# Performance work log

Measured on AMD Instinct MI355X. Metric: run time of the kernel, lower is better.

## Reference

```python
import jax, jax.numpy as jnp
import numpy as np

DT = 0.1
NUM_STEPS = 10
THRESHOLD = 0.3


def setup_inputs() -> dict:
    key = jax.random.key(0)
    k1, k2, k3 = jax.random.split(key, 3)
    B, T, D = 8, 4096, 1024
    L, O = 3, 4
    x = jax.random.normal(k1, (B, T, D), dtype=jnp.float32)
    # nn.Linear(dim, O, bias=False) weights per level, stacked: (L, O, D)
    W = jax.random.normal(k2, (L, O, D), dtype=jnp.float32) / np.sqrt(D)
    # omegas init: randn*0.1 + freq_scales[min(i,2)], freq_scales=[4.0,2.0,0.6]
    freq = jnp.array([4.0, 2.0, 0.6], dtype=jnp.float32)[:, None]
    omegas = jax.random.normal(k3, (L, O), dtype=jnp.float32) * 0.1 + freq
    # coupling strengths: 1.0 + i*0.5
    Ks = 1.0 + 0.5 * jnp.arange(L, dtype=jnp.float32)
    return {"x": x, "W": W, "omegas": omegas, "Ks": Ks}


def reference(x, W, omegas, Ks):
    B, T, D = x.shape
    L, O, _ = W.shape
    two_pi = 2.0 * jnp.pi

    # per-level projection: (L, B, T, O)
    proj = jnp.einsum('btd,lod->lbto', x, W)
    # initial phases from adjacent oscillator ratio
    phases = jnp.arctan2(proj, jnp.roll(proj, 1, axis=-1) + 1e-8) % two_pi

    om = omegas[:, None, None, :]      # (L,1,1,O)
    K = Ks[:, None, None, None]        # (L,1,1,1)

    def step(ph, _):
        # mean phase over time dim per oscillator (circular mean)
        mean_phase = jnp.arctan2(jnp.sin(ph).mean(axis=2, keepdims=True),
                                 jnp.cos(ph).mean(axis=2, keepdims=True))
        coupling = K * jnp.sin(mean_phase - ph) / T
        return (ph + DT * (om + coupling)) % two_pi, None

    phases, _ = jax.lax.scan(step, phases, None, length=NUM_STEPS)

    s = jnp.sin(phases)
    c = jnp.cos(phases)
    # global coherence: |mean_t exp(i*phi)| averaged over oscillators -> (B, L)
    level_coherences = jnp.sqrt(s.mean(axis=2) ** 2 + c.mean(axis=2) ** 2).mean(-1).T

    # sliding window-of-3 coherence along T -> (L, B, T-2)
    ms = (s[:, :, :-2] + s[:, :, 1:-1] + s[:, :, 2:]) / 3.0
    mc = (c[:, :, :-2] + c[:, :, 1:-1] + c[:, :, 2:]) / 3.0
    coh = jnp.sqrt(ms ** 2 + mc ** 2).mean(-1)
    # local-minimum dip detection: boundary at coherence index i+1 (i in 1..T-5)
    cond = (coh[..., 1:-1] < coh[..., :-2] - THRESHOLD) & \
           (coh[..., 1:-1] < coh[..., 2:] - THRESHOLD)      # (L, B, T-4)
    boundary_mask = jnp.pad(cond, ((0, 0), (0, 0), (2, 0)))   # (L, B, T-2)

    return phases, level_coherences, boundary_mask
```

## Files before the change

### kernel.cpp

```cpp
#include <hip/hip_runtime.h>
#include <math.h>

#define NB 8
#define NT 4096
#define ND 1024
#define NL 3
#define NO 4
#define NLO 12
#define NROWS (NB * NT)
#define TWO_PI_D 6.283185307179586476925286766559
#define DT_D 0.1
#define NSTEPS 10
#define THRESH_D 0.3

typedef double f64x4 __attribute__((ext_vector_type(4)));

__global__ __launch_bounds__(256) void k_wprep(const float* __restrict__ W,
                                               double* __restrict__ wsWt)
{
    int i = blockIdx.x * 256 + threadIdx.x;
    if (i < 1024 * 16) {
        int k = i >> 4, col = i & 15;
        wsWt[i] = (col < NLO) ? (double)W[col * ND + k] : 0.0;
    }
}

__global__ void k_probe(int* __restrict__ probe)
{
    const int l = threadIdx.x;
    f64x4 z = {0.0, 0.0, 0.0, 0.0};
    double v = (double)(l & 15);
    f64x4 d1 = __builtin_amdgcn_mfma_f64_16x16x4f64(v, 1.0, z, 0, 0, 0);
    f64x4 d2 = __builtin_amdgcn_mfma_f64_16x16x4f64(1.0, v, z, 0, 0, 0);
#pragma unroll
    for (int n = 0; n < 4; ++n) {
        probe[(l * 4 + n) * 2 + 0] = (int)(d1[n] * 0.25 + 0.5);
        probe[(l * 4 + n) * 2 + 1] = (int)(d2[n] * 0.25 + 0.5);
    }
}

__global__ __launch_bounds__(256) void k_proj(
    const float* __restrict__ x, const double* __restrict__ wsWt,
    const int* __restrict__ probe, double* __restrict__ ws_proj)
{
    __shared__ float  xs[64 * 68];
    __shared__ double wl[64 * 18];
    const int tid = threadIdx.x;
    const int lane = tid & 63;
    const int wid = tid >> 6;
    const long row0 = (long)blockIdx.x * 64;

    const int rg = tid >> 2;
    const int slot = tid & 3;

    f64x4 acc = {0.0, 0.0, 0.0, 0.0};

    for (int c = 0; c < 16; ++c) {
        if (c) __syncthreads();
#pragma unroll
        for (int j = 0; j < 4; ++j) {
            float4 v = *reinterpret_cast<const float4*>(
                x + (row0 + rg) * ND + c * 64 + (slot + 4 * j) * 4);
            *reinterpret_cast<float4*>(&xs[rg * 68 + (slot + 4 * j) * 4]) = v;
        }
        const double* wtg = wsWt + (long)c * 64 * 16;
#pragma unroll
        for (int j = 0; j < 4; ++j) {
            int idx = tid + j * 256;
            wl[(idx >> 4) * 18 + (idx & 15)] = wtg[idx];
        }
        __syncthreads();

        const float*  xrow = &xs[(wid * 16 + (lane & 15)) * 68 + (lane >> 4)];
        const double* wrow = &wl[(lane >> 4) * 18 + (lane & 15)];
#pragma unroll
        for (int kc = 0; kc < 16; ++kc) {
            double a = (double)xrow[kc * 4];
            double b = wrow[kc * 4 * 18];
            acc = __builtin_amdgcn_mfma_f64_16x16x4f64(a, b, acc, 0, 0, 0);
        }
    }

    const int* pr = probe + lane * 8;
#pragma unroll
    for (int n = 0; n < 4; ++n) {
        int i = pr[n * 2 + 0];
        int j = pr[n * 2 + 1];
        if (j < NLO)
            ws_proj[(long)j * NROWS + row0 + wid * 16 + i] = acc[n];
    }
}

#define B_THREADS 512
#define B_ELEMS (NT / B_THREADS)

__global__ __launch_bounds__(B_THREADS) void k_kuramoto(
    const float* __restrict__ omegas, const float* __restrict__ Ks,
    const double* __restrict__ ws_proj, float* __restrict__ ws_s,
    float* __restrict__ ws_c, double* __restrict__ ws_r,
    float* __restrict__ out_ph)
{
    const int g = blockIdx.x;
    const int l = g >> 5;
    const int b = (g >> 2) & 7;
    const int o = g & 3;
    const double om = (double)omegas[l * NO + o];
    const double Kv = (double)Ks[l];
    const double dtom = DT_D * om;
    const double cKT = DT_D * Kv / (double)NT;
    double sA, cA; sincos(dtom, &sA, &cA);
    const int tid = threadIdx.x;
    const int wid = tid >> 6;
    const int lane = tid & 63;
    __shared__ double lds[16];

    const double* pA = ws_proj + (long)(l * NO + o) * NROWS + (long)b * NT;
    const double* pB = ws_proj + (long)(l * NO + ((o + 3) & 3)) * NROWS + (long)b * NT;

    double ph[B_ELEMS], s[B_ELEMS], c[B_ELEMS];
#pragma unroll
    for (int k = 0; k < B_ELEMS; ++k) {
        int t = tid + k * B_THREADS;
        double y = pA[t];
        double xx = pB[t] + 1e-8;
        double p = atan2(y, xx);
        if (p < 0.0) p += TWO_PI_D;
        ph[k] = p;
        double r2 = sqrt(y * y + xx * xx);
        if (r2 > 0.0) { s[k] = y / r2; c[k] = xx / r2; }
        else          { s[k] = 0.0;    c[k] = 1.0; }
    }

    for (int step = 0; step < NSTEPS; ++step) {
        double ts = 0.0, tc = 0.0;
#pragma unroll
        for (int k = 0; k < B_ELEMS; ++k) { ts += s[k]; tc += c[k]; }
#pragma unroll
        for (int off = 32; off > 0; off >>= 1) {
            ts += __shfl_down(ts, off);
            tc += __shfl_down(tc, off);
        }
        if (lane == 0) { lds[wid] = ts; lds[8 + wid] = tc; }
        __syncthreads();
        double S = 0.0, C = 0.0;
#pragma unroll
        for (int w = 0; w < 8; ++w) { S += lds[w]; C += lds[8 + w]; }
        double rr = sqrt(S * S + C * C);
        double sm, cm;
        if (rr > 0.0) { sm = S / rr; cm = C / rr; } else { sm = 0.0; cm = 1.0; }
#pragma unroll
        for (int k = 0; k < B_ELEMS; ++k) {
            double sv = sm * c[k] - cm * s[k];
            double eps = cKT * sv;
            double val = ph[k] + (dtom + eps);
            if (val >= TWO_PI_D) val -= TWO_PI_D;
            if (val < 0.0) val += TWO_PI_D;
            ph[k] = val;
            double sd = fma(cA, eps, sA);
            double cd = fma(-sA, eps, cA);
            double sn = fma(s[k], cd, c[k] * sd);
            double cn = fma(c[k], cd, -(s[k] * sd));
            s[k] = sn; c[k] = cn;
        }
        __syncthreads();
    }
    {
        double ts = 0.0, tc = 0.0;
#pragma unroll
        for (int k = 0; k < B_ELEMS; ++k) { ts += s[k]; tc += c[k]; }
#pragma unroll
        for (int off = 32; off > 0; off >>= 1) {
            ts += __shfl_down(ts, off);
            tc += __shfl_down(tc, off);
        }
        if (lane == 0) { lds[wid] = ts; lds[8 + wid] = tc; }
        __syncthreads();
        if (tid == 0) {
            double S = 0.0, C = 0.0;
#pragma unroll
            for (int w = 0; w < 8; ++w) { S += lds[w]; C += lds[8 + w]; }
            double Sm = S / (double)NT, Cm = C / (double)NT;
            ws_r[g] = sqrt(Sm * Sm + Cm * Cm);
        }
    }
#pragma unroll
    for (int k = 0; k < B_ELEMS; ++k) {
        int t = tid + k * B_THREADS;
        long idx = (long)g * NT + t;
        ws_s[idx] = (float)s[k]; ws_c[idx] = (float)c[k];
        out_ph[((long)(l * NB + b) * NT + t) * NO + o] = (float)ph[k];
    }
}

__global__ __launch_bounds__(256) void k_mask(
    const float* __restrict__ ws_s, const float* __restrict__ ws_c,
    float* __restrict__ out_mask)
{
    const int bid = blockIdx.x;
    const int lb = bid >> 4;
    const int t0 = ((bid & 15) << 8) + threadIdx.x;
    float* mrow = out_mask + (long)lb * (NT - 2);
    if ((bid & 15) == 0 && threadIdx.x < 2) mrow[threadIdx.x] = 0.0f;
    if (t0 >= NT - 4) return;
    double q[3] = {0.0, 0.0, 0.0};
#pragma unroll
    for (int o = 0; o < NO; ++o) {
        const float* ps = ws_s + ((long)lb * NO + o) * NT + t0;
        const float* pc = ws_c + ((long)lb * NO + o) * NT + t0;
        double sv[5], cv[5];
#pragma unroll
        for (int j = 0; j < 5; ++j) { sv[j] = (double)ps[j]; cv[j] = (double)pc[j]; }
#pragma unroll
        for (int j = 0; j < 3; ++j) {
            double ms = ((sv[j] + sv[j + 1]) + sv[j + 2]) / 3.0;
            double mc = ((cv[j] + cv[j + 1]) + cv[j + 2]) / 3.0;
            q[j] += sqrt(ms * ms + mc * mc);
        }
    }
    double coh0 = q[0] / 4.0, coh1 = q[1] / 4.0, coh2 = q[2] / 4.0;
    bool cond = (coh1 < coh0 - THRESH_D) && (coh1 < coh2 - THRESH_D);
    mrow[2 + t0] = cond ? 1.0f : 0.0f;
}

__global__ void k_level(const double* __restrict__ ws_r, float* __restrict__ out_lvl)
{
    const int tid = threadIdx.x;
    if (tid < NB * NL) {
        const int b = tid / NL, l = tid % NL;
        const double* r = ws_r + (long)(l * NB + b) * NO;
        double m = (((r[0] + r[1]) + r[2]) + r[3]) / 4.0;
        out_lvl[tid] = (float)m;
    }
}

extern "C" void kernel_launch(void* const* d_in, const int* in_sizes, int n_in,
                              void* d_out, int out_size, void* d_ws, size_t ws_size,
                              hipStream_t stream)
{
    const float* x      = (const float*)d_in[0];
    const float* W      = (const float*)d_in[1];
    const float* omegas = (const float*)d_in[2];
    const float* Ks     = (const float*)d_in[3];
    float* out = (float*)d_out;

    double* wsWt    = (double*)d_ws;
    double* ws_proj = wsWt + 1024 * 16;
    float*  ws_s    = (float*)(ws_proj + (long)NLO * NROWS);
    float*  ws_c    = ws_s + (long)NLO * NB * NT;
    double* ws_r    = (double*)(ws_c + (long)NLO * NB * NT);
    int*    probe   = (int*)(ws_r + 96);

    float* out_ph   = out;
    float* out_lvl  = out + 393216;
    float* out_mask = out + 393240;

    k_wprep<<<64, 256, 0, stream>>>(W, wsWt);
    k_probe<<<1, 64, 0, stream>>>(probe);
    k_proj<<<NROWS / 64, 256, 0, stream>>>(x, wsWt, probe, ws_proj);
    k_kuramoto<<<NL * NB * NO, B_THREADS, 0, stream>>>(omegas, Ks, ws_proj, ws_s, ws_c, ws_r, out_ph);
    k_mask<<<24 * 16, 256, 0, stream>>>(ws_s, ws_c, out_mask);
    k_level<<<1, 64, 0, stream>>>(ws_r, out_lvl);
}
```

Baseline: 72.30 us.

## Split projection K across warps with LDS reduction and inline MFMA layout probe

The projection kernel now uses 512-thread blocks over 32 rows. Each pair of warps covers a quarter of the 1024-long reduction dimension, and the partial accumulators are combined through shared memory at the end. Weights are read straight from global memory with register double-buffering instead of being staged in LDS, and the separate probe kernel is folded into the projection kernel. The aim is more parallelism and memory-level overlap per row tile and one fewer launch, at the cost of a shared-memory reduction and extra synchronisation.

```diff
diff --git a/kernel.cpp b/kernel.cpp
--- a/kernel.cpp
+++ b/kernel.cpp
@@ -25,69 +25,82 @@
     }
 }
 
-__global__ void k_probe(int* __restrict__ probe)
-{
-    const int l = threadIdx.x;
+__global__ __launch_bounds__(512, 6) void k_proj(
+    const float* __restrict__ x, const double* __restrict__ wsWt,
+    double* __restrict__ ws_proj)
+{
+    __shared__ char buf[4 * 32 * 68 * 4];
+    float*  xs  = reinterpret_cast<float*>(buf);
+    double* red = reinterpret_cast<double*>(buf);
+
+    const int tid  = threadIdx.x;
+    const int lane = tid & 63;
+    const int wid  = tid >> 6;
+    const int tile = wid & 1;
+    const int kq   = wid >> 1;
+    const long row0 = (long)blockIdx.x * 32;
+
+    f64x4 acc = {0.0, 0.0, 0.0, 0.0};
+
+    for (int r = 0; r < 4; ++r) {
+        if (r) __syncthreads();
+#pragma unroll
+        for (int p = 0; p < 4; ++p) {
+            int idx = tid + p * 512;
+            int w   = idx >> 9;
+            int row = (idx >> 4) & 31;
+            int sl  = idx & 15;
+            float4 v = *reinterpret_cast<const float4*>(
+                x + (row0 + row) * ND + w * 256 + r * 64 + sl * 4);
+            *reinterpret_cast<float4*>(&xs[(w * 32 + row) * 68 + sl * 4]) = v;
+        }
+        __syncthreads();
+
+        const float* arow =
+            &xs[(kq * 32 + tile * 16 + (lane & 15)) * 68 + (lane >> 4)];
+        const double* wb =
+            wsWt + (long)(kq * 256 + r * 64 + (lane >> 4)) * 16 + (lane & 15);
+
+        double bv[4], bn[4];
+#pragma unroll
+        for (int q = 0; q < 4; ++q) bv[q] = wb[q * 64];
+#pragma unroll
+        for (int g = 0; g < 4; ++g) {
+            if (g < 3) {
+#pragma unroll
+                for (int q = 0; q < 4; ++q) bn[q] = wb[(g * 4 + 4 + q) * 64];
+            }
+#pragma unroll
+            for (int q = 0; q < 4; ++q) {
+                double a = (double)arow[(g * 4 + q) * 4];
+                acc = __builtin_amdgcn_mfma_f64_16x16x4f64(a, bv[q], acc, 0, 0, 0);
+            }
+#pragma unroll
+            for (int q = 0; q < 4; ++q) bv[q] = bn[q];
+        }
+    }
+
     f64x4 z = {0.0, 0.0, 0.0, 0.0};
-    double v = (double)(l & 15);
-    f64x4 d1 = __builtin_amdgcn_mfma_f64_16x16x4f64(v, 1.0, z, 0, 0, 0);
-    f64x4 d2 = __builtin_amdgcn_mfma_f64_16x16x4f64(1.0, v, z, 0, 0, 0);
-#pragma unroll
-    for (int n = 0; n < 4; ++n) {
-        probe[(l * 4 + n) * 2 + 0] = (int)(d1[n] * 0.25 + 0.5);
-        probe[(l * 4 + n) * 2 + 1] = (int)(d2[n] * 0.25 + 0.5);
-    }
-}
-
-__global__ __launch_bounds__(256) void k_proj(
-    const float* __restrict__ x, const double* __restrict__ wsWt,
-    const int* __restrict__ probe, double* __restrict__ ws_proj)
-{
-    __shared__ float  xs[64 * 68];
-    __shared__ double wl[64 * 18];
-    const int tid = threadIdx.x;
-    const int lane = tid & 63;
-    const int wid = tid >> 6;
-    const long row0 = (long)blockIdx.x * 64;
-
-    const int rg = tid >> 2;
-    const int slot = tid & 3;
-
-    f64x4 acc = {0.0, 0.0, 0.0, 0.0};
-
-    for (int c = 0; c < 16; ++c) {
-        if (c) __syncthreads();
-#pragma unroll
-        for (int j = 0; j < 4; ++j) {
-            float4 v = *reinterpret_cast<const float4*>(
-                x + (row0 + rg) * ND + c * 64 + (slot + 4 * j) * 4);
-            *reinterpret_cast<float4*>(&xs[rg * 68 + (slot + 4 * j) * 4]) = v;
-        }
-        const double* wtg = wsWt + (long)c * 64 * 16;
-#pragma unroll
-        for (int j = 0; j < 4; ++j) {
-            int idx = tid + j * 256;
-            wl[(idx >> 4) * 18 + (idx & 15)] = wtg[idx];
-        }
-        __syncthreads();
-
-        const float*  xrow = &xs[(wid * 16 + (lane & 15)) * 68 + (lane >> 4)];
-        const double* wrow = &wl[(lane >> 4) * 18 + (lane & 15)];
-#pragma unroll
-        for (int kc = 0; kc < 16; ++kc) {
-            double a = (double)xrow[kc * 4];
-            double b = wrow[kc * 4 * 18];
-            acc = __builtin_amdgcn_mfma_f64_16x16x4f64(a, b, acc, 0, 0, 0);
-        }
-    }
-
-    const int* pr = probe + lane * 8;
-#pragma unroll
-    for (int n = 0; n < 4; ++n) {
-        int i = pr[n * 2 + 0];
-        int j = pr[n * 2 + 1];
-        if (j < NLO)
-            ws_proj[(long)j * NROWS + row0 + wid * 16 + i] = acc[n];
+    f64x4 d1 = __builtin_amdgcn_mfma_f64_16x16x4f64((double)(lane & 15), 1.0, z, 0, 0, 0);
+    f64x4 d2 = __builtin_amdgcn_mfma_f64_16x16x4f64(1.0, (double)(lane & 15), z, 0, 0, 0);
+
+    __syncthreads();
+#pragma unroll
+    for (int n = 0; n < 4; ++n)
+        red[(wid * 64 + lane) * 4 + n] = acc[n];
+    __syncthreads();
+    if (kq == 0) {
+#pragma unroll
+        for (int n = 0; n < 4; ++n) {
+            double v = (red[((0 + tile) * 64 + lane) * 4 + n] +
+                        red[((2 + tile) * 64 + lane) * 4 + n]) +
+                       (red[((4 + tile) * 64 + lane) * 4 + n] +
+                        red[((6 + tile) * 64 + lane) * 4 + n]);
+            int i = (int)(d1[n] * 0.25 + 0.5);
+            int j = (int)(d2[n] * 0.25 + 0.5);
+            if (j < NLO)
+                ws_proj[(long)j * NROWS + row0 + tile * 16 + i] = v;
+        }
     }
 }
 
@@ -248,15 +261,13 @@
     float*  ws_s    = (float*)(ws_proj + (long)NLO * NROWS);
     float*  ws_c    = ws_s + (long)NLO * NB * NT;
     double* ws_r    = (double*)(ws_c + (long)NLO * NB * NT);
-    int*    probe   = (int*)(ws_r + 96);
 
     float* out_ph   = out;
     float* out_lvl  = out + 393216;
     float* out_mask = out + 393240;
 
     k_wprep<<<64, 256, 0, stream>>>(W, wsWt);
-    k_probe<<<1, 64, 0, stream>>>(probe);
-    k_proj<<<NROWS / 64, 256, 0, stream>>>(x, wsWt, probe, ws_proj);
+    k_proj<<<NROWS / 32, 512, 0, stream>>>(x, wsWt, ws_proj);
     k_kuramoto<<<NL * NB * NO, B_THREADS, 0, stream>>>(omegas, Ks, ws_proj, ws_s, ws_c, ws_r, out_ph);
     k_mask<<<24 * 16, 256, 0, stream>>>(ws_s, ws_c, out_mask);
     k_level<<<1, 64, 0, stream>>>(ws_r, out_lvl);
```

Result: faster. 70.31 us (-2.8%).
